# Kernel tuning notes

Hardware: AMD Instinct MI355X
Metric: run time of the kernel (lower is better)

Reference implementation:

```python
import jax, jax.numpy as jnp
import numpy as np

WIN = (7, 7, 7)
N = WIN[0] * WIN[1] * WIN[2]   # 343 tokens per window
DIM = 192
NH = 6
HD = DIM // NH                  # 32
B = 128                         # batch * num_windows


def _relative_position_index():
    # exact replica of the torch buffer computation
    coords = np.stack(np.meshgrid(np.arange(WIN[0]), np.arange(WIN[1]), np.arange(WIN[2]), indexing='ij'))
    cf = coords.reshape(3, -1)                       # [3, N]
    rel = cf[:, :, None] - cf[:, None, :]            # [3, N, N]
    rel = rel.transpose(1, 2, 0).astype(np.int64)    # [N, N, 3]
    rel[..., 0] += WIN[0] - 1
    rel[..., 1] += WIN[1] - 1
    rel[..., 2] += WIN[2] - 1
    rel[..., 0] *= (2 * WIN[1] - 1) * (2 * WIN[2] - 1)
    rel[..., 1] *= (2 * WIN[2] - 1)
    return rel.sum(-1).astype(np.int32)              # [N, N]


def setup_inputs() -> dict:
    key = jax.random.key(0)
    k = jax.random.split(key, 8)
    table_size = (2 * WIN[0] - 1) * (2 * WIN[1] - 1) * (2 * WIN[2] - 1)  # 2197
    return {
        'x':        jax.random.normal(k[0], (B, N, DIM), jnp.float32),
        'x_1':      jax.random.normal(k[1], (B, N, DIM), jnp.float32),
        'qkv_w':    jax.random.normal(k[2], (3 * DIM, DIM), jnp.float32) * 0.02,
        'qkv_b':    jnp.zeros((3 * DIM,), jnp.float32),
        'proj_w':   jax.random.normal(k[3], (DIM, DIM), jnp.float32) * 0.02,
        'proj_b':   jnp.zeros((DIM,), jnp.float32),
        'rpb_table': jax.random.normal(k[4], (table_size, NH), jnp.float32) * 0.02,
        'rel_idx':  jnp.asarray(_relative_position_index()),
    }


def reference(x, x_1, qkv_w, qkv_b, proj_w, proj_b, rpb_table, rel_idx):
    scale = HD ** -0.5

    def qkv_proj(t):
        # [B, N, 3C] -> [3, B, nH, N, hd]
        q = (t @ qkv_w.T + qkv_b).reshape(B, N, 3, NH, HD).transpose(2, 0, 3, 1, 4)
        return q[0], q[1], q[2]

    qx, kx, vx = qkv_proj(x)
    q1, k1, v1 = qkv_proj(x_1)

    # gathered relative-position bias: [1, nH, N, N]
    bias = rpb_table[rel_idx.reshape(-1)].reshape(N, N, NH).transpose(2, 0, 1)[None]

    def attend(q, k, v):
        a = jnp.einsum('bhnd,bhmd->bhnm', q * scale, k) + bias
        a = jax.nn.softmax(a, axis=-1)
        o = jnp.einsum('bhnm,bhmd->bhnd', a, v).transpose(0, 2, 1, 3).reshape(B, N, DIM)
        return o @ proj_w.T + proj_b

    # cross-modal pairing: q from x with k,v from x_1; q from x_1 with k,v from x
    out = attend(qx, k1, v1)
    out_1 = attend(q1, kx, vx)
    return out, out_1
```

## Files before the change

### kernel.cpp

```cpp
#include <hip/hip_runtime.h>
#include <hip/hip_bf16.h>

#define BW 128
#define NTOK 343
#define DIMC 192
#define NHEAD 6
#define HDIM 32
#define TOK (BW * NTOK)
#define M2 (2 * TOK)
#define NN (NTOK * NTOK)
#define BSTR 344
#define BNN (NTOK * BSTR)
#define QSCALE 0.17677669529663687f
#define LOG2E 1.4426950408889634f

typedef unsigned int uint32;
typedef __attribute__((ext_vector_type(8))) short short8;
typedef __attribute__((ext_vector_type(4))) float f32x4;

__device__ __forceinline__ unsigned short f2bf(float f) {
  uint32 u = __float_as_uint(f);
  u += 0x7fffu + ((u >> 16) & 1u);
  return (unsigned short)(u >> 16);
}

__device__ __forceinline__ uint32 pkpair(float a, float b) {
  __hip_bfloat162 h = __float22bfloat162_rn(make_float2(a, b));
  uint32 u;
  __builtin_memcpy(&u, &h, 4);
  return u;
}

__device__ __forceinline__ uint4 pack8bf(const float4 a, const float4 b) {
  uint4 pk;
  pk.x = pkpair(a.x, a.y);
  pk.y = pkpair(a.z, a.w);
  pk.z = pkpair(b.x, b.y);
  pk.w = pkpair(b.z, b.w);
  return pk;
}

__device__ __forceinline__ float fexp2(float x) {
  float r;
  asm("v_exp_f32 %0, %1" : "=v"(r) : "v"(x));
  return r;
}

__device__ __forceinline__ int vperm(int n) {
  const int base = n & ~31, l = n & 31, lo = l & 15, hi = l >> 4;
  return base + ((lo >> 2) << 3) + (hi << 2) + (lo & 3);
}

__global__ void k_bias(const float* __restrict__ rpb, const int* __restrict__ ridx,
                       float* __restrict__ biasws) {
  const int idx = blockIdx.x * 256 + threadIdx.x;
  if (idx < NN) {
    const int r = ridx[idx];
    const int i = idx / NTOK, j = idx % NTOK;
#pragma unroll
    for (int h = 0; h < NHEAD; ++h)
      biasws[h * BNN + i * BSTR + j] = rpb[r * NHEAD + h] * LOG2E;
  }
}

__global__ __launch_bounds__(256) void k_qkv(const float* __restrict__ x,
                                             const float* __restrict__ x1,
                                             const float* __restrict__ w,
                                             const float* __restrict__ bvec,
                                             unsigned short* __restrict__ qkvo) {
  __shared__ unsigned short Xs[128][200];
  __shared__ unsigned short Ws[64][200];
  const int R0 = blockIdx.x * 128;
  const int s = R0 / TOK;
  const int tokbase = R0 % TOK;
  const float* __restrict__ src = s ? x1 : x;
  const int tid = threadIdx.x;
  const int lane = tid & 63, wv = tid >> 6;
  const int c16 = lane & 15, q4 = lane >> 4;
  const int wr = wv >> 1, wc = wv & 1;

  int bidxv[4], nnv[4];
#pragma unroll
  for (int n = 0; n < 4; ++n) {
    const int tok = tokbase + wr * 64 + n * 16 + c16;
    bidxv[n] = tok / NTOK;
    nnv[n] = tok % NTOK;
  }

  for (int c = tid; c < 128 * 24; c += 256) {
    const int r = c / 24, k8 = (c % 24) * 8;
    const float* p = &src[(size_t)(tokbase + r) * DIMC + k8];
    const float4 a = *reinterpret_cast<const float4*>(p);
    const float4 b = *reinterpret_cast<const float4*>(p + 4);
    *reinterpret_cast<uint4*>(&Xs[r][k8]) = pack8bf(a, b);
  }

  float4 wa[6], wb[6];
#pragma unroll
  for (int i = 0; i < 6; ++i) {
    const int c = tid + i * 256;
    const int r = c / 24, k8 = (c % 24) * 8;
    const float* p = &w[(size_t)r * DIMC + k8];
    wa[i] = *reinterpret_cast<const float4*>(p);
    wb[i] = *reinterpret_cast<const float4*>(p + 4);
  }

  for (int ct = 0; ct < 9; ++ct) {
    __syncthreads();
#pragma unroll
    for (int i = 0; i < 6; ++i) {
      const int c = tid + i * 256;
      const int r = c / 24, k8 = (c % 24) * 8;
      *reinterpret_cast<uint4*>(&Ws[r][k8]) = pack8bf(wa[i], wb[i]);
    }
    __syncthreads();

    if (ct < 8) {
#pragma unroll
      for (int i = 0; i < 6; ++i) {
        const int c = tid + i * 256;
        const int r = c / 24, k8 = (c % 24) * 8;
        const float* p = &w[(size_t)((ct + 1) * 64 + r) * DIMC + k8];
        wa[i] = *reinterpret_cast<const float4*>(p);
        wb[i] = *reinterpret_cast<const float4*>(p + 4);
      }
    }

    const int colbase = ct * 64 + wc * 32;
    f32x4 acc[2][4];
#pragma unroll
    for (int m = 0; m < 2; ++m) {
      const float4 bb = *reinterpret_cast<const float4*>(&bvec[colbase + m * 16 + q4 * 4]);
#pragma unroll
      for (int n = 0; n < 4; ++n) acc[m][n] = f32x4{bb.x, bb.y, bb.z, bb.w};
    }
#pragma unroll
    for (int ks = 0; ks < 6; ++ks) {
      const short8 w0 = *reinterpret_cast<const short8*>(&Ws[wc * 32 + c16][ks * 32 + q4 * 8]);
      const short8 w1 = *reinterpret_cast<const short8*>(&Ws[wc * 32 + 16 + c16][ks * 32 + q4 * 8]);
      short8 xf[4];
#pragma unroll
      for (int n = 0; n < 4; ++n)
        xf[n] = *reinterpret_cast<const short8*>(&Xs[wr * 64 + n * 16 + c16][ks * 32 + q4 * 8]);
#pragma unroll
      for (int n = 0; n < 4; ++n) {
        acc[0][n] = __builtin_amdgcn_mfma_f32_16x16x32_bf16(w0, xf[n], acc[0][n], 0, 0, 0);
        acc[1][n] = __builtin_amdgcn_mfma_f32_16x16x32_bf16(w1, xf[n], acc[1][n], 0, 0, 0);
      }
    }

    const int t = ct / 3;
    const float qs = (t == 0) ? (QSCALE * LOG2E) : 1.0f;
#pragma unroll
    for (int m = 0; m < 2; ++m) {
      const int col0 = colbase + m * 16 + q4 * 4;
      const int h = (col0 - t * DIMC) / HDIM;
      const int d0 = col0 & (HDIM - 1);
      const size_t hb = ((size_t)(s * 3 + t) * BW) * NHEAD + h;
#pragma unroll
      for (int n = 0; n < 4; ++n) {
        const f32x4 a = acc[m][n];
        uint2 pk;
        pk.x = pkpair(a[0] * qs, a[1] * qs);
        pk.y = pkpair(a[2] * qs, a[3] * qs);
        const size_t ob = ((hb + (size_t)bidxv[n] * NHEAD) * NTOK + nnv[n]) * HDIM + d0;
        *reinterpret_cast<uint2*>(&qkvo[ob]) = pk;
      }
    }
  }
}

__global__ __launch_bounds__(512) void k_attn(const __hip_bfloat16* __restrict__ qkvi,
                                              const float* __restrict__ biasws,
                                              __hip_bfloat16* __restrict__ Ows) {
  __shared__ unsigned short Ks[352][40];
  __shared__ unsigned short Vt[32][360];
  const int bid = blockIdx.x;
  const int h = bid / (2 * BW);
  const int sb = bid % (2 * BW);
  const int s = sb >> 7;
  const int b = sb & 127;
  const int so = 1 - s;
  const size_t qbase = (((size_t)(s * 3 + 0) * BW + b) * NHEAD + h) * (size_t)NTOK * HDIM;
  const size_t kbase = (((size_t)(so * 3 + 1) * BW + b) * NHEAD + h) * (size_t)NTOK * HDIM;
  const size_t vbase = (((size_t)(so * 3 + 2) * BW + b) * NHEAD + h) * (size_t)NTOK * HDIM;
  const unsigned short* __restrict__ qp = (const unsigned short*)qkvi;
  unsigned short* __restrict__ op = (unsigned short*)Ows;
  const float* __restrict__ bh = biasws + (size_t)h * BNN;
  const int tid = threadIdx.x;

  for (int idx = tid; idx < 352 * 4; idx += 512) {
    const int n = idx >> 2, d0 = (idx & 3) * 8;
    uint4 v = {0u, 0u, 0u, 0u};
    if (n < NTOK) v = *reinterpret_cast<const uint4*>(qp + kbase + (size_t)n * HDIM + d0);
    *reinterpret_cast<uint4*>(&Ks[n][d0]) = v;
  }
  for (int idx = tid; idx < NTOK * 4; idx += 512) {
    const int n = idx >> 2, d0 = (idx & 3) * 8;
    const int np = vperm(n);
    const uint4 v = *reinterpret_cast<const uint4*>(qp + vbase + (size_t)n * HDIM + d0);
    const unsigned short* ep = reinterpret_cast<const unsigned short*>(&v);
#pragma unroll
    for (int e = 0; e < 8; ++e) Vt[d0 + e][np] = ep[e];
  }
  for (int idx = tid; idx < 32 * 9; idx += 512)
    Vt[idx / 9][vperm(NTOK + idx % 9)] = 0;
  __syncthreads();

  const int lane = tid & 63, w = tid >> 6;
  const int c16 = lane & 15, q4 = lane >> 4;
  const bool loSel = (q4 < 2);

  for (int qt = w; qt < 22; qt += 8) {
    const int iq = qt * 16 + c16;
    const int iqc = (iq < NTOK) ? iq : NTOK - 1;
    const short8 qf = *reinterpret_cast<const short8*>(qp + qbase + (size_t)iqc * HDIM + q4 * 8);
    const float* brow = bh + (size_t)iqc * BSTR;

    f32x4 o0 = {0.f, 0.f, 0.f, 0.f}, o1 = {0.f, 0.f, 0.f, 0.f};
    float mA, sumA;

    {
      f32x4 acc[12];
#pragma unroll
      for (int kt = 0; kt < 12; ++kt) {
        const float4 bv = *reinterpret_cast<const float4*>(brow + kt * 16 + q4 * 4);
        acc[kt] = f32x4{bv.x, bv.y, bv.z, bv.w};
      }
      __builtin_amdgcn_s_setprio(1);
#pragma unroll
      for (int kt = 0; kt < 12; ++kt) {
        const short8 kf = *reinterpret_cast<const short8*>(&Ks[kt * 16 + c16][q4 * 8]);
        acc[kt] = __builtin_amdgcn_mfma_f32_16x16x32_bf16(kf, qf, acc[kt], 0, 0, 0);
      }
      __builtin_amdgcn_s_setprio(0);
      float m0 = acc[0][0], m1 = acc[0][1], m2 = acc[0][2], m3 = acc[0][3];
#pragma unroll
      for (int kt = 1; kt < 12; ++kt) {
        m0 = fmaxf(m0, acc[kt][0]);
        m1 = fmaxf(m1, acc[kt][1]);
        m2 = fmaxf(m2, acc[kt][2]);
        m3 = fmaxf(m3, acc[kt][3]);
      }
      float m = fmaxf(fmaxf(m0, m1), fmaxf(m2, m3));
      m = fmaxf(m, __shfl_xor(m, 16, 64));
      m = fmaxf(m, __shfl_xor(m, 32, 64));
      mA = m;
      float s0 = 0.f, s1 = 0.f, s2 = 0.f, s3 = 0.f;
#pragma unroll
      for (int kt = 0; kt < 12; ++kt) {
        const float p0 = fexp2(acc[kt][0] - m); acc[kt][0] = p0; s0 += p0;
        const float p1 = fexp2(acc[kt][1] - m); acc[kt][1] = p1; s1 += p1;
        const float p2 = fexp2(acc[kt][2] - m); acc[kt][2] = p2; s2 += p2;
        const float p3 = fexp2(acc[kt][3] - m); acc[kt][3] = p3; s3 += p3;
      }
      sumA = (s0 + s1) + (s2 + s3);

      __builtin_amdgcn_s_setprio(1);
#pragma unroll
      for (int ks = 0; ks < 6; ++ks) {
        uint4 pw;
        pw.x = pkpair(acc[2 * ks][0], acc[2 * ks][1]);
        pw.y = pkpair(acc[2 * ks][2], acc[2 * ks][3]);
        pw.z = pkpair(acc[2 * ks + 1][0], acc[2 * ks + 1][1]);
        pw.w = pkpair(acc[2 * ks + 1][2], acc[2 * ks + 1][3]);
        const short8 pf = *reinterpret_cast<const short8*>(&pw);
        const short8 v0 = *reinterpret_cast<const short8*>(&Vt[c16][ks * 32 + q4 * 8]);
        const short8 v1 = *reinterpret_cast<const short8*>(&Vt[16 + c16][ks * 32 + q4 * 8]);
        o0 = __builtin_amdgcn_mfma_f32_16x16x32_bf16(pf, v0, o0, 0, 0, 0);
        o1 = __builtin_amdgcn_mfma_f32_16x16x32_bf16(pf, v1, o1, 0, 0, 0);
      }
      __builtin_amdgcn_s_setprio(0);
    }

    float rinv;
    {
      f32x4 acc[10];
#pragma unroll
      for (int k2 = 0; k2 < 10; ++k2) {
        const int kt = 12 + k2;
        const int jb = (kt < 21) ? (kt * 16 + q4 * 4) : (336 + (loSel ? q4 * 4 : 0));
        const float4 bv = *reinterpret_cast<const float4*>(brow + jb);
        acc[k2] = f32x4{bv.x, bv.y, bv.z, bv.w};
      }
      __builtin_amdgcn_s_setprio(1);
#pragma unroll
      for (int k2 = 0; k2 < 10; ++k2) {
        const short8 kf = *reinterpret_cast<const short8*>(&Ks[(12 + k2) * 16 + c16][q4 * 8]);
        acc[k2] = __builtin_amdgcn_mfma_f32_16x16x32_bf16(kf, qf, acc[k2], 0, 0, 0);
      }
      __builtin_amdgcn_s_setprio(0);
#pragma unroll
      for (int r = 0; r < 4; ++r)
        if (q4 * 4 + r >= 7) acc[9][r] = -1e30f;

      float m0 = acc[0][0], m1 = acc[0][1], m2 = acc[0][2], m3 = acc[0][3];
#pragma unroll
      for (int k2 = 1; k2 < 10; ++k2) {
        m0 = fmaxf(m0, acc[k2][0]);
        m1 = fmaxf(m1, acc[k2][1]);
        m2 = fmaxf(m2, acc[k2][2]);
        m3 = fmaxf(m3, acc[k2][3]);
      }
      float m = fmaxf(fmaxf(m0, m1), fmaxf(m2, m3));
      m = fmaxf(m, __shfl_xor(m, 16, 64));
      m = fmaxf(m, __shfl_xor(m, 32, 64));
      m = fmaxf(m, mA);
      const float alpha = fexp2(mA - m);

      float s0 = 0.f, s1 = 0.f, s2 = 0.f, s3 = 0.f;
#pragma unroll
      for (int k2 = 0; k2 < 10; ++k2) {
        const float p0 = fexp2(acc[k2][0] - m); acc[k2][0] = p0; s0 += p0;
        const float p1 = fexp2(acc[k2][1] - m); acc[k2][1] = p1; s1 += p1;
        const float p2 = fexp2(acc[k2][2] - m); acc[k2][2] = p2; s2 += p2;
        const float p3 = fexp2(acc[k2][3] - m); acc[k2][3] = p3; s3 += p3;
      }
      float lanesum = sumA * alpha + ((s0 + s1) + (s2 + s3));
      lanesum += __shfl_xor(lanesum, 16, 64);
      lanesum += __shfl_xor(lanesum, 32, 64);
      rinv = 1.f / lanesum;

      float alphar[4];
#pragma unroll
      for (int r = 0; r < 4; ++r) alphar[r] = __shfl(alpha, q4 * 4 + r, 64);
#pragma unroll
      for (int r = 0; r < 4; ++r) {
        o0[r] *= alphar[r];
        o1[r] *= alphar[r];
      }

      __builtin_amdgcn_s_setprio(1);
#pragma unroll
      for (int ks = 6; ks < 11; ++ks) {
        const int k2 = 2 * (ks - 6);
        uint4 pw;
        pw.x = pkpair(acc[k2][0], acc[k2][1]);
        pw.y = pkpair(acc[k2][2], acc[k2][3]);
        pw.z = pkpair(acc[k2 + 1][0], acc[k2 + 1][1]);
        pw.w = pkpair(acc[k2 + 1][2], acc[k2 + 1][3]);
        const short8 pf = *reinterpret_cast<const short8*>(&pw);
        const short8 v0 = *reinterpret_cast<const short8*>(&Vt[c16][ks * 32 + q4 * 8]);
        const short8 v1 = *reinterpret_cast<const short8*>(&Vt[16 + c16][ks * 32 + q4 * 8]);
        o0 = __builtin_amdgcn_mfma_f32_16x16x32_bf16(pf, v0, o0, 0, 0, 0);
        o1 = __builtin_amdgcn_mfma_f32_16x16x32_bf16(pf, v1, o1, 0, 0, 0);
      }
      __builtin_amdgcn_s_setprio(0);
    }

    float rsv[4];
#pragma unroll
    for (int r = 0; r < 4; ++r) rsv[r] = __shfl(rinv, q4 * 4 + r, 64);
#pragma unroll
    for (int r = 0; r < 4; ++r) {
      const int i = qt * 16 + q4 * 4 + r;
      if (i < NTOK) {
        const size_t ob = ((size_t)s * TOK + (size_t)b * NTOK + i) * DIMC + h * HDIM;
        op[ob + c16]      = f2bf(o0[r] * rsv[r]);
        op[ob + 16 + c16] = f2bf(o1[r] * rsv[r]);
      }
    }
  }
}

__global__ __launch_bounds__(256) void k_proj(const unsigned short* __restrict__ Oin,
                                              const float* __restrict__ w,
                                              const float* __restrict__ pb,
                                              float* __restrict__ out) {
  __shared__ unsigned short Xs[64][200];
  __shared__ unsigned short Ws[64][200];
  const int R0 = blockIdx.x * 64;
  const int tid = threadIdx.x;
  const int lane = tid & 63, wv = tid >> 6;
  const int c16 = lane & 15, q4 = lane >> 4;
  const int wr = wv >> 1, wc = wv & 1;

  for (int c = tid; c < 64 * 24; c += 256) {
    const int r = c / 24, k8 = (c % 24) * 8;
    *reinterpret_cast<uint4*>(&Xs[r][k8]) =
        *reinterpret_cast<const uint4*>(&Oin[(size_t)(R0 + r) * DIMC + k8]);
  }

  for (int ct = 0; ct < 3; ++ct) {
    __syncthreads();
    for (int c = tid; c < 64 * 24; c += 256) {
      const int r = c / 24, k8 = (c % 24) * 8;
      const float* p = &w[(size_t)(ct * 64 + r) * DIMC + k8];
      const float4 a = *reinterpret_cast<const float4*>(p);
      const float4 b = *reinterpret_cast<const float4*>(p + 4);
      *reinterpret_cast<uint4*>(&Ws[r][k8]) = pack8bf(a, b);
    }
    __syncthreads();

    const int colbase = ct * 64 + wc * 32;
    f32x4 acc[2][2];
#pragma unroll
    for (int m = 0; m < 2; ++m) {
      const float4 bb = *reinterpret_cast<const float4*>(&pb[colbase + m * 16 + q4 * 4]);
      acc[m][0] = f32x4{bb.x, bb.y, bb.z, bb.w};
      acc[m][1] = f32x4{bb.x, bb.y, bb.z, bb.w};
    }
#pragma unroll
    for (int ks = 0; ks < 6; ++ks) {
      const short8 x0 = *reinterpret_cast<const short8*>(&Xs[wr * 32 + c16][ks * 32 + q4 * 8]);
      const short8 x1f = *reinterpret_cast<const short8*>(&Xs[wr * 32 + 16 + c16][ks * 32 + q4 * 8]);
      const short8 w0 = *reinterpret_cast<const short8*>(&Ws[wc * 32 + c16][ks * 32 + q4 * 8]);
      const short8 w1 = *reinterpret_cast<const short8*>(&Ws[wc * 32 + 16 + c16][ks * 32 + q4 * 8]);
      acc[0][0] = __builtin_amdgcn_mfma_f32_16x16x32_bf16(w0, x0, acc[0][0], 0, 0, 0);
      acc[0][1] = __builtin_amdgcn_mfma_f32_16x16x32_bf16(w0, x1f, acc[0][1], 0, 0, 0);
      acc[1][0] = __builtin_amdgcn_mfma_f32_16x16x32_bf16(w1, x0, acc[1][0], 0, 0, 0);
      acc[1][1] = __builtin_amdgcn_mfma_f32_16x16x32_bf16(w1, x1f, acc[1][1], 0, 0, 0);
    }

#pragma unroll
    for (int m = 0; m < 2; ++m) {
      const int col0 = colbase + m * 16 + q4 * 4;
#pragma unroll
      for (int n = 0; n < 2; ++n) {
        const int row = R0 + wr * 32 + n * 16 + c16;
        float4 ov;
        ov.x = acc[m][n][0];
        ov.y = acc[m][n][1];
        ov.z = acc[m][n][2];
        ov.w = acc[m][n][3];
        *reinterpret_cast<float4*>(&out[(size_t)row * DIMC + col0]) = ov;
      }
    }
  }
}

extern "C" void kernel_launch(void* const* d_in, const int* in_sizes, int n_in,
                              void* d_out, int out_size, void* d_ws, size_t ws_size,
                              hipStream_t stream) {
  const float* x      = (const float*)d_in[0];
  const float* x1     = (const float*)d_in[1];
  const float* qkv_w  = (const float*)d_in[2];
  const float* qkv_b  = (const float*)d_in[3];
  const float* proj_w = (const float*)d_in[4];
  const float* proj_b = (const float*)d_in[5];
  const float* rpb    = (const float*)d_in[6];
  const int*   ridx   = (const int*)d_in[7];
  float* out = (float*)d_out;

  char* ws = (char*)d_ws;
  unsigned short* qkv  = (unsigned short*)ws;
  unsigned short* Ows  = (unsigned short*)(ws + 101154816);
  float*          bws  = (float*)(ws + 101154816 + 33718272);

  k_bias<<<(NN + 255) / 256, 256, 0, stream>>>(rpb, ridx, bws);
  k_qkv<<<M2 / 128, 256, 0, stream>>>(x, x1, qkv_w, qkv_b, qkv);
  k_attn<<<2 * BW * NHEAD, 512, 0, stream>>>((const __hip_bfloat16*)qkv, bws,
                                             (__hip_bfloat16*)Ows);
  k_proj<<<M2 / 64, 256, 0, stream>>>(Ows, proj_w, proj_b, out);
}
```

Baseline: 176.0 us.

## Enlarge proj row tile, register-prefetch weight chunks, hoist attention bias loads

```diff
diff --git a/kernel.cpp b/kernel.cpp
--- a/kernel.cpp
+++ b/kernel.cpp
@@ -217,6 +217,14 @@
     const short8 qf = *reinterpret_cast<const short8*>(qp + qbase + (size_t)iqc * HDIM + q4 * 8);
     const float* brow = bh + (size_t)iqc * BSTR;
 
+    float4 bB[10];
+#pragma unroll
+    for (int k2 = 0; k2 < 10; ++k2) {
+      const int kt = 12 + k2;
+      const int jb = (kt < 21) ? (kt * 16 + q4 * 4) : (336 + (loSel ? q4 * 4 : 0));
+      bB[k2] = *reinterpret_cast<const float4*>(brow + jb);
+    }
+
     f32x4 o0 = {0.f, 0.f, 0.f, 0.f}, o1 = {0.f, 0.f, 0.f, 0.f};
     float mA, sumA;
 
@@ -277,12 +285,8 @@
     {
       f32x4 acc[10];
 #pragma unroll
-      for (int k2 = 0; k2 < 10; ++k2) {
-        const int kt = 12 + k2;
-        const int jb = (kt < 21) ? (kt * 16 + q4 * 4) : (336 + (loSel ? q4 * 4 : 0));
-        const float4 bv = *reinterpret_cast<const float4*>(brow + jb);
-        acc[k2] = f32x4{bv.x, bv.y, bv.z, bv.w};
-      }
+      for (int k2 = 0; k2 < 10; ++k2)
+        acc[k2] = f32x4{bB[k2].x, bB[k2].y, bB[k2].z, bB[k2].w};
       __builtin_amdgcn_s_setprio(1);
 #pragma unroll
       for (int k2 = 0; k2 < 10; ++k2) {
@@ -367,57 +371,80 @@
                                               const float* __restrict__ w,
                                               const float* __restrict__ pb,
                                               float* __restrict__ out) {
-  __shared__ unsigned short Xs[64][200];
+  __shared__ unsigned short Xs[128][200];
   __shared__ unsigned short Ws[64][200];
-  const int R0 = blockIdx.x * 64;
+  const int R0 = blockIdx.x * 128;
   const int tid = threadIdx.x;
   const int lane = tid & 63, wv = tid >> 6;
   const int c16 = lane & 15, q4 = lane >> 4;
   const int wr = wv >> 1, wc = wv & 1;
 
-  for (int c = tid; c < 64 * 24; c += 256) {
+  for (int c = tid; c < 128 * 24; c += 256) {
     const int r = c / 24, k8 = (c % 24) * 8;
     *reinterpret_cast<uint4*>(&Xs[r][k8]) =
         *reinterpret_cast<const uint4*>(&Oin[(size_t)(R0 + r) * DIMC + k8]);
   }
 
+  float4 wa[6], wb[6];
+#pragma unroll
+  for (int i = 0; i < 6; ++i) {
+    const int c = tid + i * 256;
+    const int r = c / 24, k8 = (c % 24) * 8;
+    const float* p = &w[(size_t)r * DIMC + k8];
+    wa[i] = *reinterpret_cast<const float4*>(p);
+    wb[i] = *reinterpret_cast<const float4*>(p + 4);
+  }
+
   for (int ct = 0; ct < 3; ++ct) {
     __syncthreads();
-    for (int c = tid; c < 64 * 24; c += 256) {
+#pragma unroll
+    for (int i = 0; i < 6; ++i) {
+      const int c = tid + i * 256;
       const int r = c / 24, k8 = (c % 24) * 8;
-      const float* p = &w[(size_t)(ct * 64 + r) * DIMC + k8];
-      const float4 a = *reinterpret_cast<const float4*>(p);
-      const float4 b = *reinterpret_cast<const float4*>(p + 4);
-      *reinterpret_cast<uint4*>(&Ws[r][k8]) = pack8bf(a, b);
+      *reinterpret_cast<uint4*>(&Ws[r][k8]) = pack8bf(wa[i], wb[i]);
     }
     __syncthreads();
 
+    if (ct < 2) {
+#pragma unroll
+      for (int i = 0; i < 6; ++i) {
+        const int c = tid + i * 256;
+        const int r = c / 24, k8 = (c % 24) * 8;
+        const float* p = &w[(size_t)((ct + 1) * 64 + r) * DIMC + k8];
+        wa[i] = *reinterpret_cast<const float4*>(p);
+        wb[i] = *reinterpret_cast<const float4*>(p + 4);
+      }
+    }
+
     const int colbase = ct * 64 + wc * 32;
-    f32x4 acc[2][2];
+    f32x4 acc[2][4];
 #pragma unroll
     for (int m = 0; m < 2; ++m) {
       const float4 bb = *reinterpret_cast<const float4*>(&pb[colbase + m * 16 + q4 * 4]);
-      acc[m][0] = f32x4{bb.x, bb.y, bb.z, bb.w};
-      acc[m][1] = f32x4{bb.x, bb.y, bb.z, bb.w};
+#pragma unroll
+      for (int n = 0; n < 4; ++n) acc[m][n] = f32x4{bb.x, bb.y, bb.z, bb.w};
     }
 #pragma unroll
     for (int ks = 0; ks < 6; ++ks) {
-      const short8 x0 = *reinterpret_cast<const short8*>(&Xs[wr * 32 + c16][ks * 32 + q4 * 8]);
-      const short8 x1f = *reinterpret_cast<const short8*>(&Xs[wr * 32 + 16 + c16][ks * 32 + q4 * 8]);
       const short8 w0 = *reinterpret_cast<const short8*>(&Ws[wc * 32 + c16][ks * 32 + q4 * 8]);
       const short8 w1 = *reinterpret_cast<const short8*>(&Ws[wc * 32 + 16 + c16][ks * 32 + q4 * 8]);
-      acc[0][0] = __builtin_amdgcn_mfma_f32_16x16x32_bf16(w0, x0, acc[0][0], 0, 0, 0);
-      acc[0][1] = __builtin_amdgcn_mfma_f32_16x16x32_bf16(w0, x1f, acc[0][1], 0, 0, 0);
-      acc[1][0] = __builtin_amdgcn_mfma_f32_16x16x32_bf16(w1, x0, acc[1][0], 0, 0, 0);
-      acc[1][1] = __builtin_amdgcn_mfma_f32_16x16x32_bf16(w1, x1f, acc[1][1], 0, 0, 0);
+      short8 xf[4];
+#pragma unroll
+      for (int n = 0; n < 4; ++n)
+        xf[n] = *reinterpret_cast<const short8*>(&Xs[wr * 64 + n * 16 + c16][ks * 32 + q4 * 8]);
+#pragma unroll
+      for (int n = 0; n < 4; ++n) {
+        acc[0][n] = __builtin_amdgcn_mfma_f32_16x16x32_bf16(w0, xf[n], acc[0][n], 0, 0, 0);
+        acc[1][n] = __builtin_amdgcn_mfma_f32_16x16x32_bf16(w1, xf[n], acc[1][n], 0, 0, 0);
+      }
     }
 
 #pragma unroll
     for (int m = 0; m < 2; ++m) {
       const int col0 = colbase + m * 16 + q4 * 4;
 #pragma unroll
-      for (int n = 0; n < 2; ++n) {
-        const int row = R0 + wr * 32 + n * 16 + c16;
+      for (int n = 0; n < 4; ++n) {
+        const int row = R0 + wr * 64 + n * 16 + c16;
         float4 ov;
         ov.x = acc[m][n][0];
         ov.y = acc[m][n][1];
@@ -451,5 +478,5 @@
   k_qkv<<<M2 / 128, 256, 0, stream>>>(x, x1, qkv_w, qkv_b, qkv);
   k_attn<<<2 * BW * NHEAD, 512, 0, stream>>>((const __hip_bfloat16*)qkv, bws,
                                              (__hip_bfloat16*)Ows);
-  k_proj<<<M2 / 64, 256, 0, stream>>>(Ows, proj_w, proj_b, out);
-}
+  k_proj<<<M2 / 128, 256, 0, stream>>>(Ows, proj_w, proj_b, out);
+}
```

After: 184.0 us. 4.5% more time.
